# Kernel tuning notes

Hardware: AMD Instinct MI355X
Metric: run time of the kernel (lower is better)

The kernel has to match this reference:

```python
import jax, jax.numpy as jnp
import numpy as np

B, H, T, D = 4, 16, 2048, 128

def setup_inputs() -> dict:
    key = jax.random.key(0)
    kq, kk, kv = jax.random.split(key, 3)
    q = jax.random.normal(kq, (B, H, T, D), dtype=jnp.float32)
    k = jax.random.normal(kk, (B, H, T, D), dtype=jnp.float32)
    v = jax.random.normal(kv, (B, H, T, D), dtype=jnp.float32)
    return {"q": q, "k": k, "v": v}

def reference(q, k, v):
    # scores: [B,H,T,T] = q @ k^T, masked multiplicatively by causal lower-tri ones
    T_ = q.shape[-2]
    mask = jnp.tril(jnp.ones((T_, T_), dtype=q.dtype))  # CausalMulMask
    scores = jnp.einsum('bhid,bhjd->bhij', q, k) * mask
    # no softmax: linear attention, scores @ v
    return jnp.einsum('bhij,bhjd->bhid', scores, v)
```

## Files before the change

### kernel.cpp

```cpp
#include <hip/hip_runtime.h>
#include <stdint.h>

#define SEQ    2048
#define DIM    128
#define CHUNK  128
#define NCHUNK 16
#define NBH    64
#define DSPLIT 4
#define DCOLS  32

typedef __attribute__((ext_vector_type(8))) short short8;
typedef __attribute__((ext_vector_type(4))) float floatx4;

#define MFMA(a, b, c) __builtin_amdgcn_mfma_f32_16x16x32_bf16((a), (b), (c), 0, 0, 0)

__device__ __forceinline__ short f2bf(float f) {
  union { float f; uint32_t u; } x; x.f = f;
  uint32_t r = x.u + 0x7fffu + ((x.u >> 16) & 1u);
  return (short)(r >> 16);
}
__device__ __forceinline__ short8 pack8(const float4 a, const float4 b) {
  short8 s;
  s[0] = f2bf(a.x); s[1] = f2bf(a.y); s[2] = f2bf(a.z); s[3] = f2bf(a.w);
  s[4] = f2bf(b.x); s[5] = f2bf(b.y); s[6] = f2bf(b.z); s[7] = f2bf(b.w);
  return s;
}

__global__ __launch_bounds__(512, 2) void k_fused(
    const float* __restrict__ qin, const float* __restrict__ kin,
    const float* __restrict__ vin, float* __restrict__ out) {
  const int blk = blockIdx.x;
  const int bh  = blk & 63;
  const int dsl = blk >> 6;
  const int ds0 = dsl * DCOLS;
  const size_t hb = (size_t)bh * SEQ * DIM;
  const float* qb = qin + hb;
  const float* kb = kin + hb;
  const float* vb = vin + hb;
  float* ob = out + hb;

  __shared__ short Klds[128][136];
  __shared__ short Vt[32][136];
  __shared__ short Stl[32][136];
  __shared__ short Ps[128][136];

  const int tid  = threadIdx.x;
  const int wave = tid >> 6;
  const int lane = tid & 63;
  const int q4   = lane >> 4;
  const int l16  = lane & 15;

  floatx4 stacc[2];
#pragma unroll
  for (int mt = 0; mt < 2; ++mt)
#pragma unroll
    for (int r = 0; r < 4; ++r) stacc[mt][r] = 0.f;

  float4 qx[4][2], kx[4][2], vx[2];
  const int vj = tid >> 3, vd0 = (tid & 7) * 4;

  auto load_chunk = [&](int c) {
    const float* qrow = qb + (size_t)c * CHUNK * DIM
                        + (size_t)(wave * 16 + l16) * DIM + q4 * 8;
#pragma unroll
    for (int ks = 0; ks < 4; ++ks) {
      qx[ks][0] = *(const float4*)(qrow + ks * 32);
      qx[ks][1] = *(const float4*)(qrow + ks * 32 + 4);
    }
    const float* kcp = kb + (size_t)c * CHUNK * DIM;
#pragma unroll
    for (int it = 0; it < 4; ++it) {
      const int e = it * 4096 + tid * 8;
      kx[it][0] = *(const float4*)(kcp + e);
      kx[it][1] = *(const float4*)(kcp + e + 4);
    }
    const float* vcp = vb + (size_t)c * CHUNK * DIM + ds0;
    vx[0] = *(const float4*)(vcp + (size_t)vj * DIM + vd0);
    vx[1] = *(const float4*)(vcp + (size_t)(vj + 64) * DIM + vd0);
  };

  load_chunk(0);

  for (int c = 0; c < NCHUNK; ++c) {
    __syncthreads();

#pragma unroll
    for (int it = 0; it < 4; ++it) {
      const int e = it * 4096 + tid * 8;
      *(short8*)&Klds[e >> 7][e & 127] = pack8(kx[it][0], kx[it][1]);
    }
    Vt[vd0 + 0][vj] = f2bf(vx[0].x);
    Vt[vd0 + 1][vj] = f2bf(vx[0].y);
    Vt[vd0 + 2][vj] = f2bf(vx[0].z);
    Vt[vd0 + 3][vj] = f2bf(vx[0].w);
    Vt[vd0 + 0][vj + 64] = f2bf(vx[1].x);
    Vt[vd0 + 1][vj + 64] = f2bf(vx[1].y);
    Vt[vd0 + 2][vj + 64] = f2bf(vx[1].z);
    Vt[vd0 + 3][vj + 64] = f2bf(vx[1].w);
#pragma unroll
    for (int mt = 0; mt < 2; ++mt)
#pragma unroll
      for (int r = 0; r < 4; ++r)
        Stl[mt * 16 + q4 * 4 + r][wave * 16 + l16] = f2bf(stacc[mt][r]);

    short8 aq[4];
#pragma unroll
    for (int ks = 0; ks < 4; ++ks) aq[ks] = pack8(qx[ks][0], qx[ks][1]);

    __syncthreads();

    if (c + 1 < NCHUNK) load_chunk(c + 1);

    floatx4 oacc[2];
#pragma unroll
    for (int tn = 0; tn < 2; ++tn)
#pragma unroll
      for (int r = 0; r < 4; ++r) oacc[tn][r] = 0.f;
#pragma unroll
    for (int ks = 0; ks < 4; ++ks)
#pragma unroll
      for (int tn = 0; tn < 2; ++tn) {
        const short8 bs = *(const short8*)&Stl[tn * 16 + l16][ks * 32 + q4 * 8];
        oacc[tn] = MFMA(aq[ks], bs, oacc[tn]);
      }

    for (int tj = 0; tj <= wave; ++tj) {
      floatx4 sacc;
#pragma unroll
      for (int r = 0; r < 4; ++r) sacc[r] = 0.f;
#pragma unroll
      for (int ks = 0; ks < 4; ++ks) {
        const short8 bk = *(const short8*)&Klds[tj * 16 + l16][ks * 32 + q4 * 8];
        sacc = MFMA(aq[ks], bk, sacc);
      }
#pragma unroll
      for (int r = 0; r < 4; ++r) {
        float val = sacc[r];
        if (tj == wave && l16 > q4 * 4 + r) val = 0.f;
        Ps[wave * 16 + q4 * 4 + r][tj * 16 + l16] = f2bf(val);
      }
    }
    if ((wave & 1) == 0) {
#pragma unroll
      for (int r = 0; r < 4; ++r)
        Ps[wave * 16 + q4 * 4 + r][(wave + 1) * 16 + l16] = 0;
    }

    const int kst = (wave + 2) >> 1;
    for (int t = 0; t < kst; ++t) {
      const short8 ap = *(const short8*)&Ps[wave * 16 + l16][t * 32 + q4 * 8];
#pragma unroll
      for (int tn = 0; tn < 2; ++tn) {
        const short8 bv = *(const short8*)&Vt[tn * 16 + l16][t * 32 + q4 * 8];
        oacc[tn] = MFMA(ap, bv, oacc[tn]);
      }
    }

    float* oc = ob + (size_t)c * CHUNK * DIM;
#pragma unroll
    for (int tn = 0; tn < 2; ++tn)
#pragma unroll
      for (int r = 0; r < 4; ++r)
        oc[(size_t)(wave * 16 + q4 * 4 + r) * DIM + ds0 + tn * 16 + l16] =
            oacc[tn][r];

#pragma unroll
    for (int ks = 0; ks < 4; ++ks) {
      short8 bkc;
#pragma unroll
      for (int r = 0; r < 8; ++r)
        bkc[r] = Klds[ks * 32 + q4 * 8 + r][wave * 16 + l16];
#pragma unroll
      for (int mt = 0; mt < 2; ++mt) {
        const short8 av = *(const short8*)&Vt[mt * 16 + l16][ks * 32 + q4 * 8];
        stacc[mt] = MFMA(av, bkc, stacc[mt]);
      }
    }
  }
}

extern "C" void kernel_launch(void* const* d_in, const int* in_sizes, int n_in,
                              void* d_out, int out_size, void* d_ws, size_t ws_size,
                              hipStream_t stream) {
  const float* q = (const float*)d_in[0];
  const float* k = (const float*)d_in[1];
  const float* v = (const float*)d_in[2];
  float* out = (float*)d_out;
  (void)d_ws; (void)ws_size; (void)in_sizes; (void)n_in; (void)out_size;

  hipLaunchKernelGGL(k_fused, dim3(NBH * DSPLIT), dim3(512), 0, stream,
                     q, k, v, out);
}
```

Measured before the change: 246.7 us.

## Split fused linear attention into state-prefix kernel and per-chunk output kernel

Replaces the single sequential-over-chunks kernel with two launches. The first computes running K^T V prefix states per chunk (split over value columns) and writes them as bf16 to workspace. The second launches one block per (head, chunk), loads the prefix state and computes the intra-chunk causal part plus the inter-chunk contribution, giving far more parallel blocks. It adds a workspace round trip, a second launch, and redundant Q/K/V reads, and relies on workspace being large enough.

```diff
diff --git a/kernel.cpp b/kernel.cpp
--- a/kernel.cpp
+++ b/kernel.cpp
@@ -6,8 +6,8 @@
 #define CHUNK  128
 #define NCHUNK 16
 #define NBH    64
-#define DSPLIT 4
-#define DCOLS  32
+#define DSLA   4
+#define DCA    32
 
 typedef __attribute__((ext_vector_type(8))) short short8;
 typedef __attribute__((ext_vector_type(4))) float floatx4;
@@ -26,157 +26,217 @@
   return s;
 }
 
-__global__ __launch_bounds__(512, 2) void k_fused(
-    const float* __restrict__ qin, const float* __restrict__ kin,
-    const float* __restrict__ vin, float* __restrict__ out) {
+__global__ __launch_bounds__(512, 2) void k_state(
+    const float* __restrict__ kin, const float* __restrict__ vin,
+    short* __restrict__ ws) {
   const int blk = blockIdx.x;
   const int bh  = blk & 63;
   const int dsl = blk >> 6;
-  const int ds0 = dsl * DCOLS;
-  const size_t hb = (size_t)bh * SEQ * DIM;
-  const float* qb = qin + hb;
-  const float* kb = kin + hb;
-  const float* vb = vin + hb;
-  float* ob = out + hb;
-
-  __shared__ short Klds[128][136];
-  __shared__ short Vt[32][136];
-  __shared__ short Stl[32][136];
-  __shared__ short Ps[128][136];
+  const int ds0 = dsl * DCA;
+  const float* kb = kin + (size_t)bh * SEQ * DIM;
+  const float* vb = vin + (size_t)bh * SEQ * DIM;
+
+  __shared__ short Kt[128][136];
+  __shared__ short Vt[DCA][136];
+  __shared__ short Ss[DCA][136];
 
   const int tid  = threadIdx.x;
   const int wave = tid >> 6;
   const int lane = tid & 63;
   const int q4   = lane >> 4;
   const int l16  = lane & 15;
-
-  floatx4 stacc[2];
+  const int j    = tid & 127;
+  const int dhi  = tid >> 7;
+
+  floatx4 acc[2];
 #pragma unroll
   for (int mt = 0; mt < 2; ++mt)
 #pragma unroll
-    for (int r = 0; r < 4; ++r) stacc[mt][r] = 0.f;
-
-  float4 qx[4][2], kx[4][2], vx[2];
-  const int vj = tid >> 3, vd0 = (tid & 7) * 4;
-
-  auto load_chunk = [&](int c) {
-    const float* qrow = qb + (size_t)c * CHUNK * DIM
-                        + (size_t)(wave * 16 + l16) * DIM + q4 * 8;
-#pragma unroll
-    for (int ks = 0; ks < 4; ++ks) {
-      qx[ks][0] = *(const float4*)(qrow + ks * 32);
-      qx[ks][1] = *(const float4*)(qrow + ks * 32 + 4);
-    }
-    const float* kcp = kb + (size_t)c * CHUNK * DIM;
+    for (int r = 0; r < 4; ++r) acc[mt][r] = 0.f;
+
+  float4 kreg[4][2], vreg[2];
+  auto load_c = [&](int c) {
+    const float* krow = kb + (size_t)(c * CHUNK + j) * DIM + dhi * 8;
 #pragma unroll
     for (int it = 0; it < 4; ++it) {
-      const int e = it * 4096 + tid * 8;
-      kx[it][0] = *(const float4*)(kcp + e);
-      kx[it][1] = *(const float4*)(kcp + e + 4);
-    }
-    const float* vcp = vb + (size_t)c * CHUNK * DIM + ds0;
-    vx[0] = *(const float4*)(vcp + (size_t)vj * DIM + vd0);
-    vx[1] = *(const float4*)(vcp + (size_t)(vj + 64) * DIM + vd0);
+      kreg[it][0] = *(const float4*)(krow + it * 32);
+      kreg[it][1] = *(const float4*)(krow + it * 32 + 4);
+    }
+    const float* vrow = vb + (size_t)(c * CHUNK + j) * DIM + ds0 + dhi * 8;
+    vreg[0] = *(const float4*)(vrow);
+    vreg[1] = *(const float4*)(vrow + 4);
   };
-
-  load_chunk(0);
+  load_c(0);
 
   for (int c = 0; c < NCHUNK; ++c) {
     __syncthreads();
 
 #pragma unroll
     for (int it = 0; it < 4; ++it) {
-      const int e = it * 4096 + tid * 8;
-      *(short8*)&Klds[e >> 7][e & 127] = pack8(kx[it][0], kx[it][1]);
-    }
-    Vt[vd0 + 0][vj] = f2bf(vx[0].x);
-    Vt[vd0 + 1][vj] = f2bf(vx[0].y);
-    Vt[vd0 + 2][vj] = f2bf(vx[0].z);
-    Vt[vd0 + 3][vj] = f2bf(vx[0].w);
-    Vt[vd0 + 0][vj + 64] = f2bf(vx[1].x);
-    Vt[vd0 + 1][vj + 64] = f2bf(vx[1].y);
-    Vt[vd0 + 2][vj + 64] = f2bf(vx[1].z);
-    Vt[vd0 + 3][vj + 64] = f2bf(vx[1].w);
+      const int d0 = it * 32 + dhi * 8;
+      Kt[d0 + 0][j] = f2bf(kreg[it][0].x);
+      Kt[d0 + 1][j] = f2bf(kreg[it][0].y);
+      Kt[d0 + 2][j] = f2bf(kreg[it][0].z);
+      Kt[d0 + 3][j] = f2bf(kreg[it][0].w);
+      Kt[d0 + 4][j] = f2bf(kreg[it][1].x);
+      Kt[d0 + 5][j] = f2bf(kreg[it][1].y);
+      Kt[d0 + 6][j] = f2bf(kreg[it][1].z);
+      Kt[d0 + 7][j] = f2bf(kreg[it][1].w);
+    }
+    {
+      const int d0 = dhi * 8;
+      Vt[d0 + 0][j] = f2bf(vreg[0].x);
+      Vt[d0 + 1][j] = f2bf(vreg[0].y);
+      Vt[d0 + 2][j] = f2bf(vreg[0].z);
+      Vt[d0 + 3][j] = f2bf(vreg[0].w);
+      Vt[d0 + 4][j] = f2bf(vreg[1].x);
+      Vt[d0 + 5][j] = f2bf(vreg[1].y);
+      Vt[d0 + 6][j] = f2bf(vreg[1].z);
+      Vt[d0 + 7][j] = f2bf(vreg[1].w);
+    }
 #pragma unroll
     for (int mt = 0; mt < 2; ++mt)
 #pragma unroll
       for (int r = 0; r < 4; ++r)
-        Stl[mt * 16 + q4 * 4 + r][wave * 16 + l16] = f2bf(stacc[mt][r]);
-
-    short8 aq[4];
-#pragma unroll
-    for (int ks = 0; ks < 4; ++ks) aq[ks] = pack8(qx[ks][0], qx[ks][1]);
+        Ss[mt * 16 + q4 * 4 + r][wave * 16 + l16] = f2bf(acc[mt][r]);
 
     __syncthreads();
 
-    if (c + 1 < NCHUNK) load_chunk(c + 1);
-
-    floatx4 oacc[2];
-#pragma unroll
-    for (int tn = 0; tn < 2; ++tn)
-#pragma unroll
-      for (int r = 0; r < 4; ++r) oacc[tn][r] = 0.f;
+    if (c + 1 < NCHUNK) load_c(c + 1);
+
+    {
+      const int ks2 = tid >> 7, tnl = (tid >> 6) & 1;
+      const int q42 = (tid >> 4) & 3, l162 = tid & 15;
+      const short8 sv = *(const short8*)&Ss[tnl * 16 + l162][ks2 * 32 + q42 * 8];
+      *(short8*)&ws[((size_t)((bh * 16 + c) * 4 + dsl)) * 4096 + (size_t)tid * 8] = sv;
+    }
+
+#pragma unroll
+    for (int ks = 0; ks < 4; ++ks) {
+      const short8 bk = *(const short8*)&Kt[wave * 16 + l16][ks * 32 + q4 * 8];
+#pragma unroll
+      for (int mt = 0; mt < 2; ++mt) {
+        const short8 av = *(const short8*)&Vt[mt * 16 + l16][ks * 32 + q4 * 8];
+        acc[mt] = MFMA(av, bk, acc[mt]);
+      }
+    }
+  }
+}
+
+__global__ __launch_bounds__(512, 2) void k_out(
+    const float* __restrict__ qin, const float* __restrict__ kin,
+    const float* __restrict__ vin, const short* __restrict__ ws,
+    float* __restrict__ out) {
+  const int blk = blockIdx.x;
+  const int bh  = blk & 63;
+  const int c   = blk >> 6;
+  const size_t base = (size_t)bh * SEQ * DIM + (size_t)c * CHUNK * DIM;
+  const float* qc = qin + base;
+  const float* kc = kin + base;
+  const float* vc = vin + base;
+  float* oc = out + base;
+
+  __shared__ short Klds[128][136];
+  __shared__ short Vt[128][136];
+  __shared__ short Ps[128][136];
+  __shared__ short Sb[16384];
+
+  const int tid  = threadIdx.x;
+  const int wave = tid >> 6;
+  const int lane = tid & 63;
+  const int q4   = lane >> 4;
+  const int l16  = lane & 15;
+  const int j    = tid & 127;
+  const int dhi  = tid >> 7;
+
+  const float* qrow = qc + (size_t)(wave * 16 + l16) * DIM + q4 * 8;
+  short8 aq[4];
+#pragma unroll
+  for (int ks = 0; ks < 4; ++ks)
+    aq[ks] = pack8(*(const float4*)(qrow + ks * 32),
+                   *(const float4*)(qrow + ks * 32 + 4));
+
+#pragma unroll
+  for (int it = 0; it < 4; ++it) {
+    const int e = it * 4096 + tid * 8;
+    *(short8*)&Klds[e >> 7][e & 127] =
+        pack8(*(const float4*)(kc + e), *(const float4*)(kc + e + 4));
+  }
+#pragma unroll
+  for (int it = 0; it < 4; ++it) {
+    const int d0 = it * 32 + dhi * 8;
+    const float* vrow = vc + (size_t)j * DIM + d0;
+    const float4 a = *(const float4*)vrow;
+    const float4 b = *(const float4*)(vrow + 4);
+    Vt[d0 + 0][j] = f2bf(a.x); Vt[d0 + 1][j] = f2bf(a.y);
+    Vt[d0 + 2][j] = f2bf(a.z); Vt[d0 + 3][j] = f2bf(a.w);
+    Vt[d0 + 4][j] = f2bf(b.x); Vt[d0 + 5][j] = f2bf(b.y);
+    Vt[d0 + 6][j] = f2bf(b.z); Vt[d0 + 7][j] = f2bf(b.w);
+  }
+  if (c > 0) {
+    const short* sp = ws + (size_t)(bh * 16 + c) * 16384;
+#pragma unroll
+    for (int it = 0; it < 4; ++it) {
+      const int off = it * 4096 + tid * 8;
+      *(short8*)&Sb[off] = *(const short8*)&sp[off];
+    }
+  }
+  __syncthreads();
+
+  floatx4 oacc[8];
+#pragma unroll
+  for (int tn = 0; tn < 8; ++tn)
+#pragma unroll
+    for (int r = 0; r < 4; ++r) oacc[tn][r] = 0.f;
+
+  if (c > 0) {
 #pragma unroll
     for (int ks = 0; ks < 4; ++ks)
 #pragma unroll
-      for (int tn = 0; tn < 2; ++tn) {
-        const short8 bs = *(const short8*)&Stl[tn * 16 + l16][ks * 32 + q4 * 8];
+      for (int tn = 0; tn < 8; ++tn) {
+        const short8 bs = *(const short8*)
+            &Sb[(tn >> 1) * 4096 + ks * 1024 + (tn & 1) * 512 + lane * 8];
         oacc[tn] = MFMA(aq[ks], bs, oacc[tn]);
       }
-
-    for (int tj = 0; tj <= wave; ++tj) {
-      floatx4 sacc;
-#pragma unroll
-      for (int r = 0; r < 4; ++r) sacc[r] = 0.f;
-#pragma unroll
-      for (int ks = 0; ks < 4; ++ks) {
-        const short8 bk = *(const short8*)&Klds[tj * 16 + l16][ks * 32 + q4 * 8];
-        sacc = MFMA(aq[ks], bk, sacc);
-      }
-#pragma unroll
-      for (int r = 0; r < 4; ++r) {
-        float val = sacc[r];
-        if (tj == wave && l16 > q4 * 4 + r) val = 0.f;
-        Ps[wave * 16 + q4 * 4 + r][tj * 16 + l16] = f2bf(val);
-      }
-    }
-    if ((wave & 1) == 0) {
-#pragma unroll
-      for (int r = 0; r < 4; ++r)
-        Ps[wave * 16 + q4 * 4 + r][(wave + 1) * 16 + l16] = 0;
-    }
-
-    const int kst = (wave + 2) >> 1;
-    for (int t = 0; t < kst; ++t) {
-      const short8 ap = *(const short8*)&Ps[wave * 16 + l16][t * 32 + q4 * 8];
-#pragma unroll
-      for (int tn = 0; tn < 2; ++tn) {
-        const short8 bv = *(const short8*)&Vt[tn * 16 + l16][t * 32 + q4 * 8];
-        oacc[tn] = MFMA(ap, bv, oacc[tn]);
-      }
-    }
-
-    float* oc = ob + (size_t)c * CHUNK * DIM;
-#pragma unroll
-    for (int tn = 0; tn < 2; ++tn)
-#pragma unroll
-      for (int r = 0; r < 4; ++r)
-        oc[(size_t)(wave * 16 + q4 * 4 + r) * DIM + ds0 + tn * 16 + l16] =
-            oacc[tn][r];
-
+  }
+
+  for (int tj = 0; tj <= wave; ++tj) {
+    floatx4 sacc;
+#pragma unroll
+    for (int r = 0; r < 4; ++r) sacc[r] = 0.f;
 #pragma unroll
     for (int ks = 0; ks < 4; ++ks) {
-      short8 bkc;
-#pragma unroll
-      for (int r = 0; r < 8; ++r)
-        bkc[r] = Klds[ks * 32 + q4 * 8 + r][wave * 16 + l16];
-#pragma unroll
-      for (int mt = 0; mt < 2; ++mt) {
-        const short8 av = *(const short8*)&Vt[mt * 16 + l16][ks * 32 + q4 * 8];
-        stacc[mt] = MFMA(av, bkc, stacc[mt]);
-      }
-    }
-  }
+      const short8 bk = *(const short8*)&Klds[tj * 16 + l16][ks * 32 + q4 * 8];
+      sacc = MFMA(aq[ks], bk, sacc);
+    }
+#pragma unroll
+    for (int r = 0; r < 4; ++r) {
+      float val = sacc[r];
+      if (tj == wave && l16 > q4 * 4 + r) val = 0.f;
+      Ps[wave * 16 + q4 * 4 + r][tj * 16 + l16] = f2bf(val);
+    }
+  }
+  if ((wave & 1) == 0) {
+#pragma unroll
+    for (int r = 0; r < 4; ++r)
+      Ps[wave * 16 + q4 * 4 + r][(wave + 1) * 16 + l16] = 0;
+  }
+
+  const int kst = (wave + 2) >> 1;
+  for (int t = 0; t < kst; ++t) {
+    const short8 ap = *(const short8*)&Ps[wave * 16 + l16][t * 32 + q4 * 8];
+#pragma unroll
+    for (int tn = 0; tn < 8; ++tn) {
+      const short8 bv = *(const short8*)&Vt[tn * 16 + l16][t * 32 + q4 * 8];
+      oacc[tn] = MFMA(ap, bv, oacc[tn]);
+    }
+  }
+
+#pragma unroll
+  for (int tn = 0; tn < 8; ++tn)
+#pragma unroll
+    for (int r = 0; r < 4; ++r)
+      oc[(size_t)(wave * 16 + q4 * 4 + r) * DIM + tn * 16 + l16] = oacc[tn][r];
 }
 
 extern "C" void kernel_launch(void* const* d_in, const int* in_sizes, int n_in,
@@ -186,8 +246,10 @@
   const float* k = (const float*)d_in[1];
   const float* v = (const float*)d_in[2];
   float* out = (float*)d_out;
-  (void)d_ws; (void)ws_size; (void)in_sizes; (void)n_in; (void)out_size;
-
-  hipLaunchKernelGGL(k_fused, dim3(NBH * DSPLIT), dim3(512), 0, stream,
-                     q, k, v, out);
-}
+  (void)in_sizes; (void)n_in; (void)out_size; (void)ws_size;
+  short* ws = (short*)d_ws;
+
+  hipLaunchKernelGGL(k_state, dim3(NBH * DSLA), dim3(512), 0, stream, k, v, ws);
+  hipLaunchKernelGGL(k_out, dim3(NBH * NCHUNK), dim3(512), 0, stream,
+                     q, k, v, ws, out);
+}
```

Result: slower. 285.0 us (+15.5%).
